# Kernel tuning notes

Hardware: AMD Instinct MI355X
Metric: run time of the kernel (lower is better)

The kernel has to match this reference:

```python
import jax, jax.numpy as jnp
import numpy as np

N_NODES = 5
B, C, H, W = 4, 256, 32, 32
THRESH = 0.3
EPS = 1e-12


def setup_inputs() -> dict:
    key = jax.random.key(0)
    k1, k2, k3, k4 = jax.random.split(key, 4)
    x = jax.random.normal(k1, (N_NODES, B, C, H, W), dtype=jnp.float32)
    w = jax.random.normal(k2, (N_NODES, N_NODES), dtype=jnp.float32)
    # 5 stacked conv1x1 'experts': Conv2d(2C -> C, k=1) weight [C,2C] + bias [C]
    conv_w = jax.random.normal(k3, (N_NODES, C, 2 * C), dtype=jnp.float32) * 0.02
    conv_b = jax.random.normal(k4, (N_NODES, C), dtype=jnp.float32) * 0.02
    return {"x": x, "w": w, "conv_w": conv_w, "conv_b": conv_b}


def reference(x, w, conv_w, conv_b):
    # x: [N, B, C, H, W] -- the list of N node feature maps stacked
    N, b, c, h, ww = x.shape
    P = b * c * h * ww  # 'pixels' = total element count of one node tensor

    # conv_i(cat(node_j, node_i + node_j)) splits into W1@node_j + W2@(node_i+node_j) + b_i
    W1 = conv_w[:, :, :c]          # [N, C, C] acts on node_j
    W2 = conv_w[:, :, c:]          # [N, C, C] acts on node_i + node_j
    A = W1 + W2                    # combined weight on node_j

    term_j = jnp.einsum('ick,jbkhw->ijbchw', A, x)    # [N,N,B,C,H,W]
    term_i = jnp.einsum('ick,ibkhw->ibchw', W2, x)    # [N,B,C,H,W]
    target = term_j + term_i[:, None] + conv_b[:, None, None, :, None, None]
    distance = x[None, :] - target                    # distance[i,j] = node_j - conv_i(...)

    # edge_list[:, i, j] = flatten(distance[i, j])  -> [P, N, N]
    edge = distance.reshape(N, N, P).transpose(2, 0, 1)

    # new_edge = edge * w; sigmoid; threshold at 0.3; L2-normalize over dim=2 (j axis)
    e = jax.nn.sigmoid(edge * w)
    e = jnp.where(e > THRESH, e, jnp.zeros_like(e))
    norm = jnp.sqrt(jnp.sum(e * e, axis=2, keepdims=True))
    e = e / jnp.maximum(norm, EPS)

    # node matrix: [P, N] of flattened node features; fuse h[p,i] = sum_j e[p,i,j]*node[p,j]
    node = x.reshape(N, P).T
    hmat = jnp.einsum('pij,pj->pi', e, node)          # [P, N]
    return hmat.T.reshape(N, b, c, h, ww)
```

## Files before the change

kernel.cpp:

```cpp
#include <hip/hip_runtime.h>
#include <cmath>

#define NN  5
#define BB  4
#define CCH 256
#define HWD 1024
#define THRESH_V 0.3f
#define EPS_V 1e-12f

#define CT 32
#define WT 32
#define KC 32
#define NCHUNK (CCH / KC)
#define APAD 36
#define SPAD 36

#define SMEM_FLOATS 7424

__global__ __launch_bounds__(384)
void fub_main(const float* __restrict__ x, const float* __restrict__ wmat,
              const float* __restrict__ conv_w, const float* __restrict__ conv_b,
              float* __restrict__ out)
{
    __shared__ __align__(16) float smem[SMEM_FLOATS];
    float* Xs  = smem;
    float* As  = smem + 5120;
    float* W2s = smem + 6272;
    float* Es  = smem;

    const int tid  = threadIdx.x;
    const int wv   = tid >> 6;
    const int lane = tid & 63;

    int bid = blockIdx.x;
    const int hwt = bid & 31; bid >>= 5;
    const int b   = bid & 3;  bid >>= 2;
    const int ct  = bid & 7;  bid >>= 3;
    const int i   = bid;

    const int c0  = ct * CT;
    const int hw0 = hwt * WT;

    const int lr = (lane >> 3) << 2;
    const int lc = (lane & 7)  << 2;

    const int jx = (wv < 5) ? wv : i;
    const float* M  = (wv == 5) ? W2s : As;
    const float* Mb = M + lr;
    const float* Xb = Xs + jx * (KC * WT) + lc;

    float acc[4][4];
#pragma unroll
    for (int r = 0; r < 4; ++r)
#pragma unroll
        for (int c = 0; c < 4; ++c) acc[r][c] = 0.0f;

    const bool xloader = (tid < 320);
    float4 pfa[4];
    float4 pfb[4];

    {
        const int k0 = 0;
        if (xloader) {
#pragma unroll
            for (int it = 0; it < 4; ++it) {
                const int t   = tid + it * 320;
                const int j   = t >> 8;
                const int kk  = (t & 255) >> 3;
                const int p4  = (t & 7) << 2;
                pfa[it] = *(const float4*)(
                    x + (size_t)((j * BB + b) * CCH + k0 + kk) * HWD + hw0 + p4);
            }
        } else {
            const int u = tid - 320;
#pragma unroll
            for (int it = 0; it < 4; ++it) {
                const int t  = u + (it << 6);
                const int r  = t >> 3;
                const int kq = (t & 7) << 2;
                const float* base =
                    conv_w + (size_t)(i * CCH + c0 + r) * (2 * CCH) + k0 + kq;
                pfa[it] = *(const float4*)(base);
                pfb[it] = *(const float4*)(base + CCH);
            }
        }
    }

    for (int ch = 0; ch < NCHUNK; ++ch) {
        if (ch) __syncthreads();

        if (xloader) {
#pragma unroll
            for (int it = 0; it < 4; ++it) {
                const int t   = tid + it * 320;
                const int j   = t >> 8;
                const int kk  = (t & 255) >> 3;
                const int p4  = (t & 7) << 2;
                *(float4*)(Xs + j * (KC * WT) + kk * WT + p4) = pfa[it];
            }
        } else {
            const int u = tid - 320;
#pragma unroll
            for (int it = 0; it < 4; ++it) {
                const int t  = u + (it << 6);
                const int r  = t >> 3;
                const int kq = (t & 7) << 2;
                const float4 w1 = pfa[it];
                const float4 w2 = pfb[it];
                As [(kq + 0) * APAD + r] = w1.x + w2.x;
                As [(kq + 1) * APAD + r] = w1.y + w2.y;
                As [(kq + 2) * APAD + r] = w1.z + w2.z;
                As [(kq + 3) * APAD + r] = w1.w + w2.w;
                W2s[(kq + 0) * APAD + r] = w2.x;
                W2s[(kq + 1) * APAD + r] = w2.y;
                W2s[(kq + 2) * APAD + r] = w2.z;
                W2s[(kq + 3) * APAD + r] = w2.w;
            }
        }
        __syncthreads();

        if (ch + 1 < NCHUNK) {
            const int k0 = (ch + 1) * KC;
            if (xloader) {
#pragma unroll
                for (int it = 0; it < 4; ++it) {
                    const int t   = tid + it * 320;
                    const int j   = t >> 8;
                    const int kk  = (t & 255) >> 3;
                    const int p4  = (t & 7) << 2;
                    pfa[it] = *(const float4*)(
                        x + (size_t)((j * BB + b) * CCH + k0 + kk) * HWD + hw0 + p4);
                }
            } else {
                const int u = tid - 320;
#pragma unroll
                for (int it = 0; it < 4; ++it) {
                    const int t  = u + (it << 6);
                    const int r  = t >> 3;
                    const int kq = (t & 7) << 2;
                    const float* base =
                        conv_w + (size_t)(i * CCH + c0 + r) * (2 * CCH) + k0 + kq;
                    pfa[it] = *(const float4*)(base);
                    pfb[it] = *(const float4*)(base + CCH);
                }
            }
        }

#pragma unroll
        for (int kk = 0; kk < KC; ++kk) {
            const float4 a  = *(const float4*)(Mb + kk * APAD);
            const float4 xv = *(const float4*)(Xb + kk * WT);
            const float ar[4] = {a.x, a.y, a.z, a.w};
            const float xc[4] = {xv.x, xv.y, xv.z, xv.w};
#pragma unroll
            for (int r = 0; r < 4; ++r)
#pragma unroll
                for (int c = 0; c < 4; ++c)
                    acc[r][c] = fmaf(ar[r], xc[c], acc[r][c]);
        }
    }

    __syncthreads();
#pragma unroll
    for (int r = 0; r < 4; ++r) {
        *(float4*)(Es + wv * (CT * SPAD) + (lr + r) * SPAD + lc) =
            make_float4(acc[r][0], acc[r][1], acc[r][2], acc[r][3]);
    }
    __syncthreads();

    if (tid < 256) {
        const int row = tid >> 3;
        const int col = (tid & 7) << 2;
        const int c   = c0 + row;
        const float bias = conv_b[i * CCH + c];

        float wrow[NN];
#pragma unroll
        for (int j = 0; j < NN; ++j) wrow[j] = wmat[i * NN + j];

        const float4 T = *(const float4*)(Es + 5 * (CT * SPAD) + row * SPAD + col);
        const float Tv[4] = {T.x, T.y, T.z, T.w};

        float num[4] = {0.f, 0.f, 0.f, 0.f};
        float sq [4] = {0.f, 0.f, 0.f, 0.f};
#pragma unroll
        for (int j = 0; j < NN; ++j) {
            const float4 s  = *(const float4*)(Es + j * (CT * SPAD) + row * SPAD + col);
            const float4 xj = *(const float4*)(
                x + (size_t)((j * BB + b) * CCH + c) * HWD + hw0 + col);
            const float sv[4] = {s.x, s.y, s.z, s.w};
            const float xv[4] = {xj.x, xj.y, xj.z, xj.w};
            const float wj = wrow[j];
#pragma unroll
            for (int cc = 0; cc < 4; ++cc) {
                const float dist = xv[cc] - (sv[cc] + Tv[cc] + bias);
                const float z    = dist * wj;
                float e = 1.0f / (1.0f + __expf(-z));
                e = (e > THRESH_V) ? e : 0.0f;
                sq[cc]  = fmaf(e, e, sq[cc]);
                num[cc] = fmaf(e, xv[cc], num[cc]);
            }
        }
        float res[4];
#pragma unroll
        for (int cc = 0; cc < 4; ++cc)
            res[cc] = num[cc] / fmaxf(sqrtf(sq[cc]), EPS_V);

        *(float4*)(out + (size_t)((i * BB + b) * CCH + c) * HWD + hw0 + col) =
            make_float4(res[0], res[1], res[2], res[3]);
    }
}

extern "C" void kernel_launch(void* const* d_in, const int* in_sizes, int n_in,
                              void* d_out, int out_size, void* d_ws, size_t ws_size,
                              hipStream_t stream) {
    const float* x      = (const float*)d_in[0];
    const float* w      = (const float*)d_in[1];
    const float* conv_w = (const float*)d_in[2];
    const float* conv_b = (const float*)d_in[3];
    float* out = (float*)d_out;

    dim3 grid(5120);
    dim3 block(384);
    fub_main<<<grid, block, 0, stream>>>(x, w, conv_w, conv_b, out);
}
```

Baseline: 383.6 us.

## Enlarge block tile to 64x64 with 8x8 per-thread register microtiles

Doubles the channel and pixel tile sizes (CT/WT 32→64) and halves the K chunk to 16, so each thread accumulates an 8x8 microtile instead of 4x4. The grid shrinks from 5120 to 1280 blocks. The epilogue is split into two halves that stage results through shared memory to fit the larger tile. The aim is more FMA per shared-memory load and less redundant reloading of x and conv weights across blocks. In exchange, register pressure rises to 64 accumulators, occupancy may drop, and there are fewer blocks to spread across the GPU.

Result: slower. 495.2 us (+29.1%).

```diff
diff --git a/kernel.cpp b/kernel.cpp
--- a/kernel.cpp
+++ b/kernel.cpp
@@ -8,14 +8,14 @@
 #define THRESH_V 0.3f
 #define EPS_V 1e-12f
 
-#define CT 32
-#define WT 32
-#define KC 32
+#define CT 64
+#define WT 64
+#define KC 16
 #define NCHUNK (CCH / KC)
-#define APAD 36
-#define SPAD 36
-
-#define SMEM_FLOATS 7424
+#define APAD 68
+#define ESP 68
+
+#define SMEM_FLOATS 13056
 
 __global__ __launch_bounds__(384)
 void fub_main(const float* __restrict__ x, const float* __restrict__ wmat,
@@ -25,7 +25,7 @@
     __shared__ __align__(16) float smem[SMEM_FLOATS];
     float* Xs  = smem;
     float* As  = smem + 5120;
-    float* W2s = smem + 6272;
+    float* W2s = smem + 6208;
     float* Es  = smem;
 
     const int tid  = threadIdx.x;
@@ -33,53 +33,52 @@
     const int lane = tid & 63;
 
     int bid = blockIdx.x;
-    const int hwt = bid & 31; bid >>= 5;
+    const int hwt = bid & 15; bid >>= 4;
     const int b   = bid & 3;  bid >>= 2;
-    const int ct  = bid & 7;  bid >>= 3;
+    const int ct  = bid & 3;  bid >>= 2;
     const int i   = bid;
 
     const int c0  = ct * CT;
     const int hw0 = hwt * WT;
 
-    const int lr = (lane >> 3) << 2;
-    const int lc = (lane & 7)  << 2;
+    const int lr = (lane >> 3) << 3;
+    const int lc = (lane & 7)  << 3;
 
     const int jx = (wv < 5) ? wv : i;
-    const float* M  = (wv == 5) ? W2s : As;
-    const float* Mb = M + lr;
+    const float* Mb = ((wv == 5) ? W2s : As) + lr;
     const float* Xb = Xs + jx * (KC * WT) + lc;
 
-    float acc[4][4];
-#pragma unroll
-    for (int r = 0; r < 4; ++r)
-#pragma unroll
-        for (int c = 0; c < 4; ++c) acc[r][c] = 0.0f;
+    float acc[8][8];
+#pragma unroll
+    for (int r = 0; r < 8; ++r)
+#pragma unroll
+        for (int c = 0; c < 8; ++c) acc[r][c] = 0.0f;
 
     const bool xloader = (tid < 320);
     float4 pfa[4];
     float4 pfb[4];
 
     {
-        const int k0 = 0;
         if (xloader) {
 #pragma unroll
             for (int it = 0; it < 4; ++it) {
                 const int t   = tid + it * 320;
                 const int j   = t >> 8;
-                const int kk  = (t & 255) >> 3;
-                const int p4  = (t & 7) << 2;
+                const int rem = t & 255;
+                const int kk  = rem >> 4;
+                const int p4  = (rem & 15) << 2;
                 pfa[it] = *(const float4*)(
-                    x + (size_t)((j * BB + b) * CCH + k0 + kk) * HWD + hw0 + p4);
+                    x + (size_t)((j * BB + b) * CCH + kk) * HWD + hw0 + p4);
             }
         } else {
             const int u = tid - 320;
 #pragma unroll
             for (int it = 0; it < 4; ++it) {
-                const int t  = u + (it << 6);
-                const int r  = t >> 3;
-                const int kq = (t & 7) << 2;
+                const int f  = u + (it << 6);
+                const int r  = f >> 2;
+                const int kq = (f & 3) << 2;
                 const float* base =
-                    conv_w + (size_t)(i * CCH + c0 + r) * (2 * CCH) + k0 + kq;
+                    conv_w + (size_t)(i * CCH + c0 + r) * (2 * CCH) + kq;
                 pfa[it] = *(const float4*)(base);
                 pfb[it] = *(const float4*)(base + CCH);
             }
@@ -94,17 +93,18 @@
             for (int it = 0; it < 4; ++it) {
                 const int t   = tid + it * 320;
                 const int j   = t >> 8;
-                const int kk  = (t & 255) >> 3;
-                const int p4  = (t & 7) << 2;
+                const int rem = t & 255;
+                const int kk  = rem >> 4;
+                const int p4  = (rem & 15) << 2;
                 *(float4*)(Xs + j * (KC * WT) + kk * WT + p4) = pfa[it];
             }
         } else {
             const int u = tid - 320;
 #pragma unroll
             for (int it = 0; it < 4; ++it) {
-                const int t  = u + (it << 6);
-                const int r  = t >> 3;
-                const int kq = (t & 7) << 2;
+                const int f  = u + (it << 6);
+                const int r  = f >> 2;
+                const int kq = (f & 3) << 2;
                 const float4 w1 = pfa[it];
                 const float4 w2 = pfb[it];
                 As [(kq + 0) * APAD + r] = w1.x + w2.x;
@@ -126,8 +126,9 @@
                 for (int it = 0; it < 4; ++it) {
                     const int t   = tid + it * 320;
                     const int j   = t >> 8;
-                    const int kk  = (t & 255) >> 3;
-                    const int p4  = (t & 7) << 2;
+                    const int rem = t & 255;
+                    const int kk  = rem >> 4;
+                    const int p4  = (rem & 15) << 2;
                     pfa[it] = *(const float4*)(
                         x + (size_t)((j * BB + b) * CCH + k0 + kk) * HWD + hw0 + p4);
                 }
@@ -135,9 +136,9 @@
                 const int u = tid - 320;
 #pragma unroll
                 for (int it = 0; it < 4; ++it) {
-                    const int t  = u + (it << 6);
-                    const int r  = t >> 3;
-                    const int kq = (t & 7) << 2;
+                    const int f  = u + (it << 6);
+                    const int r  = f >> 2;
+                    const int kq = (f & 3) << 2;
                     const float* base =
                         conv_w + (size_t)(i * CCH + c0 + r) * (2 * CCH) + k0 + kq;
                     pfa[it] = *(const float4*)(base);
@@ -148,66 +149,82 @@
 
 #pragma unroll
         for (int kk = 0; kk < KC; ++kk) {
-            const float4 a  = *(const float4*)(Mb + kk * APAD);
-            const float4 xv = *(const float4*)(Xb + kk * WT);
-            const float ar[4] = {a.x, a.y, a.z, a.w};
-            const float xc[4] = {xv.x, xv.y, xv.z, xv.w};
-#pragma unroll
-            for (int r = 0; r < 4; ++r)
-#pragma unroll
-                for (int c = 0; c < 4; ++c)
+            const float4 a0 = *(const float4*)(Mb + kk * APAD);
+            const float4 a1 = *(const float4*)(Mb + kk * APAD + 4);
+            const float4 x0 = *(const float4*)(Xb + kk * WT);
+            const float4 x1 = *(const float4*)(Xb + kk * WT + 4);
+            const float ar[8] = {a0.x, a0.y, a0.z, a0.w, a1.x, a1.y, a1.z, a1.w};
+            const float xc[8] = {x0.x, x0.y, x0.z, x0.w, x1.x, x1.y, x1.z, x1.w};
+#pragma unroll
+            for (int r = 0; r < 8; ++r)
+#pragma unroll
+                for (int c = 0; c < 8; ++c)
                     acc[r][c] = fmaf(ar[r], xc[c], acc[r][c]);
         }
     }
 
-    __syncthreads();
-#pragma unroll
-    for (int r = 0; r < 4; ++r) {
-        *(float4*)(Es + wv * (CT * SPAD) + (lr + r) * SPAD + lc) =
-            make_float4(acc[r][0], acc[r][1], acc[r][2], acc[r][3]);
-    }
-    __syncthreads();
-
-    if (tid < 256) {
-        const int row = tid >> 3;
-        const int col = (tid & 7) << 2;
-        const int c   = c0 + row;
-        const float bias = conv_b[i * CCH + c];
-
-        float wrow[NN];
-#pragma unroll
-        for (int j = 0; j < NN; ++j) wrow[j] = wmat[i * NN + j];
-
-        const float4 T = *(const float4*)(Es + 5 * (CT * SPAD) + row * SPAD + col);
-        const float Tv[4] = {T.x, T.y, T.z, T.w};
-
-        float num[4] = {0.f, 0.f, 0.f, 0.f};
-        float sq [4] = {0.f, 0.f, 0.f, 0.f};
-#pragma unroll
-        for (int j = 0; j < NN; ++j) {
-            const float4 s  = *(const float4*)(Es + j * (CT * SPAD) + row * SPAD + col);
-            const float4 xj = *(const float4*)(
-                x + (size_t)((j * BB + b) * CCH + c) * HWD + hw0 + col);
-            const float sv[4] = {s.x, s.y, s.z, s.w};
-            const float xv[4] = {xj.x, xj.y, xj.z, xj.w};
-            const float wj = wrow[j];
-#pragma unroll
-            for (int cc = 0; cc < 4; ++cc) {
-                const float dist = xv[cc] - (sv[cc] + Tv[cc] + bias);
-                const float z    = dist * wj;
-                float e = 1.0f / (1.0f + __expf(-z));
-                e = (e > THRESH_V) ? e : 0.0f;
-                sq[cc]  = fmaf(e, e, sq[cc]);
-                num[cc] = fmaf(e, xv[cc], num[cc]);
-            }
-        }
-        float res[4];
-#pragma unroll
-        for (int cc = 0; cc < 4; ++cc)
-            res[cc] = num[cc] / fmaxf(sqrtf(sq[cc]), EPS_V);
-
-        *(float4*)(out + (size_t)((i * BB + b) * CCH + c) * HWD + hw0 + col) =
-            make_float4(res[0], res[1], res[2], res[3]);
+    float wrow[NN];
+#pragma unroll
+    for (int j = 0; j < NN; ++j) wrow[j] = wmat[i * NN + j];
+
+#pragma unroll
+    for (int h = 0; h < 2; ++h) {
+        __syncthreads();
+
+        if ((lane >> 5) == h) {
+            const int er0 = lr - (h << 5);
+#pragma unroll
+            for (int r = 0; r < 8; ++r) {
+                float* p = Es + wv * (32 * ESP) + (er0 + r) * ESP + lc;
+                *(float4*)(p)     = make_float4(acc[r][0], acc[r][1], acc[r][2], acc[r][3]);
+                *(float4*)(p + 4) = make_float4(acc[r][4], acc[r][5], acc[r][6], acc[r][7]);
+            }
+        }
+        __syncthreads();
+
+        if (tid < 256) {
+            const int row  = tid >> 3;
+            const int col8 = (tid & 7) << 3;
+            const int c    = c0 + (h << 5) + row;
+            const float bias = conv_b[i * CCH + c];
+
+            const float* Tp = Es + 5 * (32 * ESP) + row * ESP + col8;
+            const float4 T0 = *(const float4*)(Tp);
+            const float4 T1 = *(const float4*)(Tp + 4);
+            const float Tv[8] = {T0.x, T0.y, T0.z, T0.w, T1.x, T1.y, T1.z, T1.w};
+
+            float num[8] = {0,0,0,0,0,0,0,0};
+            float sq [8] = {0,0,0,0,0,0,0,0};
+#pragma unroll
+            for (int j = 0; j < NN; ++j) {
+                const float* Sp = Es + j * (32 * ESP) + row * ESP + col8;
+                const float4 s0 = *(const float4*)(Sp);
+                const float4 s1 = *(const float4*)(Sp + 4);
+                const float* xp = x + (size_t)((j * BB + b) * CCH + c) * HWD + hw0 + col8;
+                const float4 xa = *(const float4*)(xp);
+                const float4 xb = *(const float4*)(xp + 4);
+                const float sv[8] = {s0.x, s0.y, s0.z, s0.w, s1.x, s1.y, s1.z, s1.w};
+                const float xv[8] = {xa.x, xa.y, xa.z, xa.w, xb.x, xb.y, xb.z, xb.w};
+                const float wj = wrow[j];
+#pragma unroll
+                for (int cc = 0; cc < 8; ++cc) {
+                    const float dist = xv[cc] - (sv[cc] + Tv[cc] + bias);
+                    const float z    = dist * wj;
+                    float e = 1.0f / (1.0f + __expf(-z));
+                    e = (e > THRESH_V) ? e : 0.0f;
+                    sq[cc]  = fmaf(e, e, sq[cc]);
+                    num[cc] = fmaf(e, xv[cc], num[cc]);
+                }
+            }
+            float res[8];
+#pragma unroll
+            for (int cc = 0; cc < 8; ++cc)
+                res[cc] = num[cc] / fmaxf(sqrtf(sq[cc]), EPS_V);
+
+            float* op = out + (size_t)((i * BB + b) * CCH + c) * HWD + hw0 + col8;
+            *(float4*)(op)     = make_float4(res[0], res[1], res[2], res[3]);
+            *(float4*)(op + 4) = make_float4(res[4], res[5], res[6], res[7]);
+        }
     }
 }
 
@@ -220,7 +237,7 @@
     const float* conv_b = (const float*)d_in[3];
     float* out = (float*)d_out;
 
-    dim3 grid(5120);
+    dim3 grid(1280);
     dim3 block(384);
     fub_main<<<grid, block, 0, stream>>>(x, w, conv_w, conv_b, out);
 }
```
